# Performance work log

Measured on AMD Instinct MI355X. Metric: run time of the kernel, lower is better.

The kernel has to match this reference:

```python
import jax, jax.numpy as jnp
import numpy as np

N = 131072      # 8192 sudoku puzzles x 16 cells
E = 1048576     # random constraint edges (avg degree 8)
HID = 64
NEG_SLOPE = 0.2


def setup_inputs() -> dict:
    key = jax.random.key(0)
    ks = jax.random.split(key, 18)
    p = lambda k, shape: jax.random.normal(k, shape, dtype=jnp.float32) * 0.05
    return {
        "x": jax.random.randint(ks[0], (N,), 0, 5),
        "edge_index": jax.random.randint(ks[1], (2, E), 0, N),
        "emb": p(ks[2], (5, HID)),
        # conv1: in 64 -> heads=4, C=64, concat
        "W1": p(ks[3], (HID, 4 * HID)),
        "a1_src": p(ks[4], (4, HID)),
        "a1_dst": p(ks[5], (4, HID)),
        "b1": p(ks[6], (4 * HID,)),
        # conv2: in 256 -> heads=4, C=64, concat
        "W2": p(ks[7], (4 * HID, 4 * HID)),
        "a2_src": p(ks[8], (4, HID)),
        "a2_dst": p(ks[9], (4, HID)),
        "b2": p(ks[10], (4 * HID,)),
        # conv3: in 256 -> heads=1, C=64, no concat
        "W3": p(ks[11], (4 * HID, HID)),
        "a3_src": p(ks[12], (1, HID)),
        "a3_dst": p(ks[13], (1, HID)),
        "b3": p(ks[14], (HID,)),
        "fc_w": p(ks[15], (HID, 5)),
        "fc_b": p(ks[16], (5,)),
    }


def gat_conv(x, src, dst, W, a_src, a_dst, b, concat):
    """PyG-style GATConv (self-loops already appended to src/dst)."""
    n = x.shape[0]
    H, C = a_src.shape
    h = (x @ W).reshape(n, H, C)                       # [N,H,C]
    alpha_s = jnp.einsum('nhc,hc->nh', h, a_src)       # [N,H]
    alpha_d = jnp.einsum('nhc,hc->nh', h, a_dst)
    e = jax.nn.leaky_relu(alpha_s[src] + alpha_d[dst], NEG_SLOPE)  # [E,H]
    # scatter-softmax over incoming edges per destination node
    e_max = jax.ops.segment_max(e, dst, num_segments=n)
    e_exp = jnp.exp(e - e_max[dst])
    denom = jax.ops.segment_sum(e_exp, dst, num_segments=n)
    alpha = e_exp / (denom[dst] + 1e-16)               # [E,H]
    msg = h[src] * alpha[:, :, None]                   # [E,H,C]
    out = jax.ops.segment_sum(msg, dst, num_segments=n)  # [N,H,C]
    out = out.reshape(n, H * C) if concat else out.mean(axis=1)
    return out + b


def reference(x, edge_index, emb, W1, a1_src, a1_dst, b1,
              W2, a2_src, a2_dst, b2, W3, a3_src, a3_dst, b3, fc_w, fc_b):
    n = x.shape[0]
    loops = jnp.arange(n)
    src = jnp.concatenate([edge_index[0], loops])  # add self-loops (PyG default)
    dst = jnp.concatenate([edge_index[1], loops])
    h = emb[x]                                                    # [N,64]
    h = jax.nn.elu(gat_conv(h, src, dst, W1, a1_src, a1_dst, b1, True))
    h = jax.nn.elu(gat_conv(h, src, dst, W2, a2_src, a2_dst, b2, True))
    h = jax.nn.elu(gat_conv(h, src, dst, W3, a3_src, a3_dst, b3, False))
    return h @ fc_w + fc_b                                        # [N,5]
```

## Files before the change

kernel.cpp:

```cpp
#include <hip/hip_runtime.h>
#include <hip/hip_bf16.h>
#include <hip/hip_fp8.h>

typedef __attribute__((ext_vector_type(8))) short short8;
typedef __attribute__((ext_vector_type(4))) short short4_t;
typedef __attribute__((ext_vector_type(4))) float floatx4;
typedef __attribute__((ext_vector_type(2))) float floatx2;

constexpr int NB  = 256;
constexpr int CAP = 6144;

__device__ __forceinline__ unsigned short f2bf(float f){
  unsigned int u = __float_as_uint(f);
  u += 0x7FFF + ((u >> 16) & 1);
  return (unsigned short)(u >> 16);
}
__device__ __forceinline__ float bf2f(unsigned short h){
  return __uint_as_float(((unsigned int)h) << 16);
}
__device__ __forceinline__ float lrelu(float x){ return x > 0.f ? x : 0.2f * x; }
__device__ __forceinline__ float eluf(float x){ return x > 0.f ? x : (__expf(x) - 1.f); }

__device__ __forceinline__ unsigned char f2fp8(float f){
  __hip_fp8_e4m3 t(f);
  return (unsigned char)t.__x;
}
__device__ __forceinline__ float fp82f(unsigned char b){
  __hip_fp8_e4m3 t;
  t.__x = (__hip_fp8_storage_t)b;
  return (float)t;
}

template<bool HI>
__device__ __forceinline__ floatx2 fp8pk2(unsigned int v){
#if defined(__has_builtin) && __has_builtin(__builtin_amdgcn_cvt_pk_f32_fp8)
  return __builtin_amdgcn_cvt_pk_f32_fp8((int)v, HI);
#else
  floatx2 r;
  constexpr int sh = HI ? 16 : 0;
  r.x = fp82f((unsigned char)((v >> sh) & 0xFF));
  r.y = fp82f((unsigned char)((v >> (sh + 8)) & 0xFF));
  return r;
#endif
}

__device__ __forceinline__ unsigned int f32x4_to_fp8(float a0, float a1, float a2, float a3){
#if defined(__has_builtin) && __has_builtin(__builtin_amdgcn_cvt_pk_fp8_f32)
  int w = 0;
  w = __builtin_amdgcn_cvt_pk_fp8_f32(a0, a1, w, false);
  w = __builtin_amdgcn_cvt_pk_fp8_f32(a2, a3, w, true);
  return (unsigned int)w;
#else
  return (unsigned int)f2fp8(a0) | ((unsigned int)f2fp8(a1) << 8) |
         ((unsigned int)f2fp8(a2) << 16) | ((unsigned int)f2fp8(a3) << 24);
#endif
}

__device__ __forceinline__ int scr512(int p){
  int q = p >> 2, s = p & 3;
  int qq = ((q & 31) << 2) | (q >> 5);
  return (qq << 2) | s;
}

__device__ __forceinline__ void gload16(const unsigned short* g, unsigned short* l){
  __builtin_amdgcn_global_load_lds(
      (const __attribute__((address_space(1))) unsigned int*)(const void*)g,
      (__attribute__((address_space(3))) unsigned int*)(void*)l,
      16, 0, 0);
}

__global__ __launch_bounds__(256) void part_prep_k(const int* __restrict__ ei, int E, int shift,
                                                   const int* __restrict__ x,
                                                   int* __restrict__ gcnt,
                                                   unsigned* __restrict__ bbuf, int PB,
                                                   const float* __restrict__ W2,
                                                   unsigned short* __restrict__ Wp2,
                                                   const float* __restrict__ W3,
                                                   unsigned short* __restrict__ Wp3,
                                                   const float* __restrict__ emb,
                                                   const float* __restrict__ W1,
                                                   const float* __restrict__ a1s,
                                                   const float* __restrict__ a1d,
                                                   float* __restrict__ T1,
                                                   float* __restrict__ wt_tab){
  int blk = blockIdx.x;
  int tid = threadIdx.x;
  if (blk < PB){
    __shared__ int hist[NB];
    __shared__ int base[NB];
    hist[tid] = 0;
    __syncthreads();
    int blk_start = blk * 4096;
    int ldmask = (1 << shift) - 1;
    unsigned word[16];
    int bkt[16], lp[16];
    #pragma unroll
    for (int k = 0; k < 16; k++){
      int i = blk_start + k * 256 + tid;
      if (i < E){
        int dst = ei[E + i];
        int s = ei[i];
        int xs = x[s];
        bkt[k] = dst >> shift;
        word[k] = (unsigned)s | ((unsigned)(dst & ldmask) << 17) | ((unsigned)xs << 26);
        lp[k] = atomicAdd(&hist[bkt[k]], 1);
      } else {
        bkt[k] = -1;
      }
    }
    __syncthreads();
    base[tid] = atomicAdd(&gcnt[tid], hist[tid]);
    __syncthreads();
    #pragma unroll
    for (int k = 0; k < 16; k++){
      if (bkt[k] >= 0){
        int b = bkt[k];
        bbuf[(size_t)b * CAP + base[b] + lp[k]] = word[k];
      }
    }
    return;
  }
  int b = blk - PB;
  if (b < 256){
    int idx = b * 256 + tid;
    int k = idx >> 8, nn = idx & 255;
    Wp2[nn * 256 + k] = f2bf(W2[idx]);
  } else if (b < 320){
    int idx = (b - 256) * 256 + tid;
    int k = idx >> 6, nn = idx & 63;
    Wp3[nn * 256 + k] = f2bf(W3[idx]);
  } else {
    __shared__ float t_lds[1280];
    __shared__ float as_l[20], ad_l[20];
    for (int i = tid; i < 1280; i += 256){
      int r = i >> 8, c = i & 255;
      float s = 0.f;
      for (int k = 0; k < 64; k++) s += emb[r * 64 + k] * W1[k * 256 + c];
      t_lds[i] = s;
      T1[i] = s;
    }
    __syncthreads();
    if (tid < 20){
      int r = tid >> 2, hh = tid & 3;
      float ss = 0.f, sd = 0.f;
      for (int c = 0; c < 64; c++){
        float f = t_lds[r * 256 + hh * 64 + c];
        ss += f * a1s[hh * 64 + c];
        sd += f * a1d[hh * 64 + c];
      }
      as_l[tid] = ss;
      ad_l[tid] = sd;
    }
    __syncthreads();
    if (tid < 100){
      int xd = tid / 20, rest = tid % 20;
      int h = rest & 3;
      wt_tab[tid] = __expf(lrelu(as_l[rest] + ad_l[xd * 4 + h]));
    }
  }
}

__global__ __launch_bounds__(256) void bscan_k(const int* __restrict__ gcnt,
                                               int* __restrict__ gbase,
                                               int* __restrict__ row_ptr, int N, int dpb){
  __shared__ int s[NB];
  int t = threadIdx.x;
  int v = gcnt[t] + dpb;
  s[t] = v;
  __syncthreads();
  #pragma unroll
  for (int off = 1; off < NB; off <<= 1){
    int u = (t >= off) ? s[t - off] : 0;
    __syncthreads();
    s[t] += u;
    __syncthreads();
  }
  gbase[t] = s[t] - v;
  if (t == NB - 1){ gbase[NB] = s[t]; row_ptr[N] = s[t]; }
}

__global__ __launch_bounds__(256) void sort_k(const unsigned* __restrict__ bbuf,
                                              const int* __restrict__ gcnt,
                                              const int* __restrict__ gbase,
                                              const int* __restrict__ x,
                                              int* __restrict__ row_ptr,
                                              int* __restrict__ sorted_src,
                                              int* __restrict__ perm,
                                              uint2* __restrict__ cnt5, int dpb){
  __shared__ int counts[512];
  __shared__ int curs[512];
  __shared__ int wsum[256];
  __shared__ int sortedL[CAP + 512];
  __shared__ int dh[64];
  __shared__ int h5[512 * 5];
  int b = blockIdx.x, tid = threadIdx.x;
  int cnt = gcnt[b];
  int dstBase = b * dpb;
  int gb = gbase[b];
  counts[tid] = 0;
  counts[tid + 256] = 0;
  for (int i = tid; i < dpb * 5; i += 256) h5[i] = 0;
  __syncthreads();
  for (int i = tid; i < cnt; i += 256){
    unsigned pw = bbuf[(size_t)b * CAP + i];
    atomicAdd(&counts[(pw >> 17) & (dpb - 1)], 1);
  }
  {
    int x0 = x[dstBase + 2 * tid];
    int x1 = x[dstBase + 2 * tid + 1];
    atomicAdd(&h5[(2 * tid) * 5 + x0], 1);
    atomicAdd(&h5[(2 * tid + 1) * 5 + x1], 1);
  }
  __syncthreads();
  int c0 = counts[2 * tid] + 1;
  int c1 = counts[2 * tid + 1] + 1;
  int sum = c0 + c1;
  wsum[tid] = sum;
  __syncthreads();
  #pragma unroll
  for (int off = 1; off < 256; off <<= 1){
    int u = (tid >= off) ? wsum[tid - off] : 0;
    __syncthreads();
    wsum[tid] += u;
    __syncthreads();
  }
  int ex = wsum[tid] - sum;
  int ro0 = ex, ro1 = ex + c0;
  curs[2 * tid] = ro0 + 1;
  curs[2 * tid + 1] = ro1 + 1;
  sortedL[ro0] = dstBase + 2 * tid;
  sortedL[ro1] = dstBase + 2 * tid + 1;
  row_ptr[dstBase + 2 * tid] = gb + ro0;
  row_ptr[dstBase + 2 * tid + 1] = gb + ro1;
  __syncthreads();
  for (int i = tid; i < cnt; i += 256){
    unsigned pw = bbuf[(size_t)b * CAP + i];
    int ldst = (pw >> 17) & (dpb - 1);
    int pos = atomicAdd(&curs[ldst], 1);
    sortedL[pos] = (int)(pw & 0x1FFFF);
    atomicAdd(&h5[ldst * 5 + (pw >> 26)], 1);
  }
  __syncthreads();
  int tot = cnt + dpb;
  for (int i = tid; i < tot; i += 256) sorted_src[gb + i] = sortedL[i];

  {
    int d0 = 2 * tid, d1 = 2 * tid + 1;
    unsigned lo0 = (unsigned)h5[d0 * 5 + 0] | ((unsigned)h5[d0 * 5 + 1] << 8) |
                   ((unsigned)h5[d0 * 5 + 2] << 16) | ((unsigned)h5[d0 * 5 + 3] << 24);
    unsigned lo1 = (unsigned)h5[d1 * 5 + 0] | ((unsigned)h5[d1 * 5 + 1] << 8) |
                   ((unsigned)h5[d1 * 5 + 2] << 16) | ((unsigned)h5[d1 * 5 + 3] << 24);
    cnt5[dstBase + d0] = make_uint2(lo0, (unsigned)h5[d0 * 5 + 4]);
    cnt5[dstBase + d1] = make_uint2(lo1, (unsigned)h5[d1 * 5 + 4]);
  }

  __syncthreads();
  if (tid < 64) dh[tid] = 0;
  __syncthreads();
  int dg0 = c0 < 63 ? c0 : 63;
  int dg1 = c1 < 63 ? c1 : 63;
  int r0 = atomicAdd(&dh[dg0], 1);
  int r1 = atomicAdd(&dh[dg1], 1);
  __syncthreads();
  if (tid == 0){
    int run = 0;
    for (int i = 0; i < 64; i++){ int c = dh[i]; dh[i] = run; run += c; }
  }
  __syncthreads();
  perm[dstBase + scr512(dh[dg0] + r0)] = dstBase + 2 * tid;
  perm[dstBase + scr512(dh[dg1] + r1)] = dstBase + 2 * tid + 1;
}

template<int BN, int MODE, bool F8OUT>
__global__ __launch_bounds__(256) void gemm_lds_k(const unsigned short* __restrict__ A,
                                                  const unsigned short* __restrict__ Wp,
                                                  void* __restrict__ Cout, int Nc,
                                                  const float* __restrict__ a_src,
                                                  const float* __restrict__ a_dst,
                                                  float* __restrict__ as_arr,
                                                  float* __restrict__ ad_arr){
  constexpr int K = 256;
  constexpr int NT = BN / 32;
  __shared__ unsigned short Alds[128 * 32];
  __shared__ unsigned short Blds[BN * 32];
  __shared__ float asl[128], adl[128];
  __shared__ float pas[128][2], pad[128][2];
  int tid = threadIdx.x;
  int w = tid >> 6, l = tid & 63;
  int r16 = l & 15, quad = l >> 4;
  int wr = w >> 1, wc = w & 1;
  int mBase = blockIdx.x * 128;
  int nBase = blockIdx.y * BN;

  if constexpr (MODE == 1){
    if (tid < 128){ asl[tid] = a_src[nBase + tid]; adl[tid] = a_dst[nBase + tid]; }
  }
  if constexpr (MODE == 2){
    if (tid < 64){ asl[tid] = a_src[tid]; adl[tid] = a_dst[tid]; }
  }

  int arow = l >> 2;
  int kcol = (l & 3) * 8;
  const unsigned short* gA0 = A + (size_t)(mBase + w * 32 + arow) * K + kcol;
  const unsigned short* gA1 = gA0 + (size_t)16 * K;
  unsigned short* lA0 = &Alds[(w * 32) * 32];
  unsigned short* lA1 = &Alds[(w * 32 + 16) * 32];
  const unsigned short* gB0;
  const unsigned short* gB1 = nullptr;
  unsigned short* lB0;
  unsigned short* lB1 = nullptr;
  if constexpr (BN == 128){
    gB0 = Wp + (size_t)(nBase + w * 32 + arow) * K + kcol;
    gB1 = gB0 + (size_t)16 * K;
    lB0 = &Blds[(w * 32) * 32];
    lB1 = &Blds[(w * 32 + 16) * 32];
  } else {
    gB0 = Wp + (size_t)(nBase + w * 16 + arow) * K + kcol;
    lB0 = &Blds[(w * 16) * 32];
  }

  floatx4 acc[4][NT];
  #pragma unroll
  for (int mt = 0; mt < 4; mt++)
    #pragma unroll
    for (int nt = 0; nt < NT; nt++){ floatx4 z = {0.f,0.f,0.f,0.f}; acc[mt][nt] = z; }

  for (int kt = 0; kt < 8; kt++){
    int ko = kt * 32;
    gload16(gA0 + ko, lA0);
    gload16(gA1 + ko, lA1);
    gload16(gB0 + ko, lB0);
    if constexpr (BN == 128) gload16(gB1 + ko, lB1);
    __syncthreads();
    short8 af[4], bfr[NT];
    #pragma unroll
    for (int mt = 0; mt < 4; mt++)
      af[mt] = *(const short8*)&Alds[(wr * 64 + mt * 16 + r16) * 32 + quad * 8];
    #pragma unroll
    for (int nt = 0; nt < NT; nt++)
      bfr[nt] = *(const short8*)&Blds[(wc * (BN / 2) + nt * 16 + r16) * 32 + quad * 8];
    #pragma unroll
    for (int mt = 0; mt < 4; mt++)
      #pragma unroll
      for (int nt = 0; nt < NT; nt++)
        acc[mt][nt] = __builtin_amdgcn_mfma_f32_16x16x32_bf16(af[mt], bfr[nt], acc[mt][nt], 0, 0, 0);
    __syncthreads();
  }

  #pragma unroll
  for (int mt = 0; mt < 4; mt++){
    #pragma unroll
    for (int nt = 0; nt < NT; nt++){
      if constexpr (F8OUT){
        unsigned int pk = f32x4_to_fp8(acc[mt][nt][0] * 64.f, acc[mt][nt][1] * 64.f,
                                       acc[mt][nt][2] * 64.f, acc[mt][nt][3] * 64.f);
        int col = nBase + wc * (BN / 2) + nt * 16 + r16;
        int row0 = mBase + wr * 64 + mt * 16 + quad * 4;
        #pragma unroll
        for (int r = 0; r < 4; r++)
          ((unsigned char*)Cout)[(size_t)(row0 + r) * Nc + col] =
              (unsigned char)((pk >> (r * 8)) & 0xFF);
      } else {
        #pragma unroll
        for (int r = 0; r < 4; r++){
          int row = mBase + wr * 64 + mt * 16 + quad * 4 + r;
          int col = nBase + wc * (BN / 2) + nt * 16 + r16;
          ((unsigned short*)Cout)[(size_t)row * Nc + col] = f2bf(acc[mt][nt][r]);
        }
      }
    }
  }
  if constexpr (MODE == 1){
    int head = (nBase + wc * 64) >> 6;
    #pragma unroll
    for (int mt = 0; mt < 4; mt++){
      #pragma unroll
      for (int r = 0; r < 4; r++){
        float ps = 0.f, pd = 0.f;
        #pragma unroll
        for (int nt = 0; nt < NT; nt++){
          float v = acc[mt][nt][r];
          int ci = wc * 64 + nt * 16 + r16;
          ps += v * asl[ci];
          pd += v * adl[ci];
        }
        ps += __shfl_xor(ps, 1, 64); ps += __shfl_xor(ps, 2, 64);
        ps += __shfl_xor(ps, 4, 64); ps += __shfl_xor(ps, 8, 64);
        pd += __shfl_xor(pd, 1, 64); pd += __shfl_xor(pd, 2, 64);
        pd += __shfl_xor(pd, 4, 64); pd += __shfl_xor(pd, 8, 64);
        if (r16 == 0){
          int row = mBase + wr * 64 + mt * 16 + quad * 4 + r;
          as_arr[row * 4 + head] = ps;
          ad_arr[row * 4 + head] = pd;
        }
      }
    }
  }
  if constexpr (MODE == 2){
    #pragma unroll
    for (int mt = 0; mt < 4; mt++){
      #pragma unroll
      for (int r = 0; r < 4; r++){
        float ps = 0.f, pd = 0.f;
        #pragma unroll
        for (int nt = 0; nt < NT; nt++){
          float v = acc[mt][nt][r];
          int ci = wc * 32 + nt * 16 + r16;
          ps += v * asl[ci];
          pd += v * adl[ci];
        }
        ps += __shfl_xor(ps, 1, 64); ps += __shfl_xor(ps, 2, 64);
        ps += __shfl_xor(ps, 4, 64); ps += __shfl_xor(ps, 8, 64);
        pd += __shfl_xor(pd, 1, 64); pd += __shfl_xor(pd, 2, 64);
        pd += __shfl_xor(pd, 4, 64); pd += __shfl_xor(pd, 8, 64);
        if (r16 == 0){
          int lr = wr * 64 + mt * 16 + quad * 4 + r;
          pas[lr][wc] = ps;
          pad[lr][wc] = pd;
        }
      }
    }
    __syncthreads();
    if (tid < 128){
      as_arr[mBase + tid] = pas[tid][0] + pas[tid][1];
      ad_arr[mBase + tid] = pad[tid][0] + pad[tid][1];
    }
  }
}


__global__ __launch_bounds__(256) void agg1_k(const int* __restrict__ x,
                                              const float* __restrict__ T1,
                                              const float* __restrict__ wt_tab,
                                              const uint2* __restrict__ cnt5,
                                              const float* __restrict__ bias,
                                              unsigned short* __restrict__ outb){
  __shared__ float t_lds[1280];
  __shared__ float wt_l[100], b_lds[256];
  __shared__ float cnt_lds[256][5];
  __shared__ int xd_lds[256];
  int tid = threadIdx.x;
  for (int i = tid; i < 1280; i += 256) t_lds[i] = T1[i];
  if (tid < 100) wt_l[tid] = wt_tab[tid];
  b_lds[tid] = bias[tid];
  int d = blockIdx.x * 256 + tid;
  uint2 cw = cnt5[d];
  xd_lds[tid] = x[d];
  cnt_lds[tid][0] = (float)(cw.x & 0xFF);
  cnt_lds[tid][1] = (float)((cw.x >> 8) & 0xFF);
  cnt_lds[tid][2] = (float)((cw.x >> 16) & 0xFF);
  cnt_lds[tid][3] = (float)(cw.x >> 24);
  cnt_lds[tid][4] = (float)(cw.y & 0xFF);
  __syncthreads();
  int w = tid >> 6, l = tid & 63;
  int head = l >> 4;
  int c0i = l * 4;
  for (int dl = w; dl < 256; dl += 4){
    int dd = blockIdx.x * 256 + dl;
    int xd20 = xd_lds[dl] * 20;
    float ws[5];
    float den = 0.f;
    #pragma unroll
    for (int v2 = 0; v2 < 5; v2++){
      float wv = wt_l[xd20 + v2 * 4 + head] * cnt_lds[dl][v2];
      ws[v2] = wv;
      den += wv;
    }
    float inv = 1.f / (den + 1e-16f);
    float num[4] = {0.f, 0.f, 0.f, 0.f};
    #pragma unroll
    for (int v2 = 0; v2 < 5; v2++){
      const float4 row = *(const float4*)&t_lds[v2 * 256 + c0i];
      num[0] += ws[v2] * row.x;
      num[1] += ws[v2] * row.y;
      num[2] += ws[v2] * row.z;
      num[3] += ws[v2] * row.w;
    }
    short4_t ov;
    #pragma unroll
    for (int j = 0; j < 4; j++)
      ov[j] = (short)f2bf(eluf(num[j] * inv + b_lds[c0i + j]));
    *(short4_t*)(outb + (size_t)dd * 256 + c0i) = ov;
  }
}


__global__ __launch_bounds__(256) void agg4_k(const unsigned char* __restrict__ h8,
                                              const float* __restrict__ as_arr,
                                              const float* __restrict__ ad_arr,
                                              const int* __restrict__ row_ptr,
                                              const int* __restrict__ sorted_src,
                                              const int* __restrict__ perm,
                                              const float* __restrict__ bias,
                                              unsigned short* __restrict__ outb){
  int tid = threadIdx.x;
  int w = tid >> 6, l = tid & 63;
  int g = l >> 4, q = l & 15;
  int d = perm[blockIdx.x * 16 + w * 4 + g];
  unsigned coff = (unsigned)(q * 16);
  int head = q >> 2;
  int start = row_ptr[d], end = row_ptr[d + 1];
  float a_d = ad_arr[d * 4 + head];
  floatx2 ac[8];
  #pragma unroll
  for (int j = 0; j < 8; j++){ floatx2 z = {0.f, 0.f}; ac[j] = z; }
  float den = 0.f;
  int e = start;
  for (; e + 3 < end; e += 4){
    unsigned s0 = (unsigned)sorted_src[e];
    unsigned s1 = (unsigned)sorted_src[e + 1];
    unsigned s2 = (unsigned)sorted_src[e + 2];
    unsigned s3 = (unsigned)sorted_src[e + 3];
    uint4 v0 = *(const uint4*)(h8 + (((size_t)s0 << 8) | coff));
    uint4 v1 = *(const uint4*)(h8 + (((size_t)s1 << 8) | coff));
    uint4 v2 = *(const uint4*)(h8 + (((size_t)s2 << 8) | coff));
    uint4 v3 = *(const uint4*)(h8 + (((size_t)s3 << 8) | coff));
    float w0 = __expf(lrelu(as_arr[(s0 << 2) + head] + a_d));
    float w1 = __expf(lrelu(as_arr[(s1 << 2) + head] + a_d));
    float w2 = __expf(lrelu(as_arr[(s2 << 2) + head] + a_d));
    float w3 = __expf(lrelu(as_arr[(s3 << 2) + head] + a_d));
    den += (w0 + w1) + (w2 + w3);
    floatx2 W0 = {w0, w0}, W1 = {w1, w1}, W2 = {w2, w2}, W3 = {w3, w3};
    ac[0] += W0 * fp8pk2<false>(v0.x) + W1 * fp8pk2<false>(v1.x)
           + W2 * fp8pk2<false>(v2.x) + W3 * fp8pk2<false>(v3.x);
    ac[1] += W0 * fp8pk2<true>(v0.x)  + W1 * fp8pk2<true>(v1.x)
           + W2 * fp8pk2<true>(v2.x)  + W3 * fp8pk2<true>(v3.x);
    ac[2] += W0 * fp8pk2<false>(v0.y) + W1 * fp8pk2<false>(v1.y)
           + W2 * fp8pk2<false>(v2.y) + W3 * fp8pk2<false>(v3.y);
    ac[3] += W0 * fp8pk2<true>(v0.y)  + W1 * fp8pk2<true>(v1.y)
           + W2 * fp8pk2<true>(v2.y)  + W3 * fp8pk2<true>(v3.y);
    ac[4] += W0 * fp8pk2<false>(v0.z) + W1 * fp8pk2<false>(v1.z)
           + W2 * fp8pk2<false>(v2.z) + W3 * fp8pk2<false>(v3.z);
    ac[5] += W0 * fp8pk2<true>(v0.z)  + W1 * fp8pk2<true>(v1.z)
           + W2 * fp8pk2<true>(v2.z)  + W3 * fp8pk2<true>(v3.z);
    ac[6] += W0 * fp8pk2<false>(v0.w) + W1 * fp8pk2<false>(v1.w)
           + W2 * fp8pk2<false>(v2.w) + W3 * fp8pk2<false>(v3.w);
    ac[7] += W0 * fp8pk2<true>(v0.w)  + W1 * fp8pk2<true>(v1.w)
           + W2 * fp8pk2<true>(v2.w)  + W3 * fp8pk2<true>(v3.w);
  }
  for (; e < end; e++){
    unsigned s = (unsigned)sorted_src[e];
    uint4 v = *(const uint4*)(h8 + (((size_t)s << 8) | coff));
    float wg = __expf(lrelu(as_arr[(s << 2) + head] + a_d));
    den += wg;
    floatx2 wv = {wg, wg};
    ac[0] += wv * fp8pk2<false>(v.x);
    ac[1] += wv * fp8pk2<true>(v.x);
    ac[2] += wv * fp8pk2<false>(v.y);
    ac[3] += wv * fp8pk2<true>(v.y);
    ac[4] += wv * fp8pk2<false>(v.z);
    ac[5] += wv * fp8pk2<true>(v.z);
    ac[6] += wv * fp8pk2<false>(v.w);
    ac[7] += wv * fp8pk2<true>(v.w);
  }
  float inv = 0.015625f / (den + 1e-16f);
  int cb = q * 16;
  float4 bv0 = *(const float4*)&bias[cb];
  float4 bv1 = *(const float4*)&bias[cb + 4];
  float4 bv2 = *(const float4*)&bias[cb + 8];
  float4 bv3 = *(const float4*)&bias[cb + 12];
  float bb[16] = {bv0.x, bv0.y, bv0.z, bv0.w, bv1.x, bv1.y, bv1.z, bv1.w,
                  bv2.x, bv2.y, bv2.z, bv2.w, bv3.x, bv3.y, bv3.z, bv3.w};
  short8 o0, o1;
  #pragma unroll
  for (int j = 0; j < 8; j++){
    float v = ((j & 1) ? ac[j >> 1].y : ac[j >> 1].x);
    o0[j] = (short)f2bf(eluf(v * inv + bb[j]));
  }
  #pragma unroll
  for (int j = 0; j < 8; j++){
    float v = ((j & 1) ? ac[4 + (j >> 1)].y : ac[4 + (j >> 1)].x);
    o1[j] = (short)f2bf(eluf(v * inv + bb[8 + j]));
  }
  *(short8*)(outb + (size_t)d * 256 + cb) = o0;
  *(short8*)(outb + (size_t)d * 256 + cb + 8) = o1;
}


__global__ __launch_bounds__(256) void agg3_k(const unsigned char* __restrict__ h8,
                                              const float* __restrict__ as_arr,
                                              const float* __restrict__ ad_arr,
                                              const int* __restrict__ row_ptr,
                                              const int* __restrict__ sorted_src,
                                              const int* __restrict__ perm,
                                              const float* __restrict__ bias,
                                              const float* __restrict__ fcw,
                                              const float* __restrict__ fcb,
                                              float* __restrict__ out){
  __shared__ float w_lds[320];
  __shared__ float fb5[5];
  int tid = threadIdx.x;
  for (int i = tid; i < 320; i += 256) w_lds[i] = fcw[i];
  if (tid < 5) fb5[tid] = fcb[tid];
  __syncthreads();
  int w = tid >> 6, l = tid & 63;
  int g = l >> 3, q = l & 7;
  int d = perm[blockIdx.x * 32 + w * 8 + g];
  unsigned coff = (unsigned)(q * 8);
  int start = row_ptr[d], end = row_ptr[d + 1];
  float a_d = ad_arr[d];
  floatx2 ac[4];
  #pragma unroll
  for (int j = 0; j < 4; j++){ floatx2 z = {0.f, 0.f}; ac[j] = z; }
  float den = 0.f;
  int e = start;
  for (; e + 3 < end; e += 4){
    unsigned s0 = (unsigned)sorted_src[e];
    unsigned s1 = (unsigned)sorted_src[e + 1];
    unsigned s2 = (unsigned)sorted_src[e + 2];
    unsigned s3 = (unsigned)sorted_src[e + 3];
    uint2 v0 = *(const uint2*)(h8 + (((size_t)s0 << 6) | coff));
    uint2 v1 = *(const uint2*)(h8 + (((size_t)s1 << 6) | coff));
    uint2 v2 = *(const uint2*)(h8 + (((size_t)s2 << 6) | coff));
    uint2 v3 = *(const uint2*)(h8 + (((size_t)s3 << 6) | coff));
    float w0 = __expf(lrelu(as_arr[s0] + a_d));
    float w1 = __expf(lrelu(as_arr[s1] + a_d));
    float w2 = __expf(lrelu(as_arr[s2] + a_d));
    float w3 = __expf(lrelu(as_arr[s3] + a_d));
    den += (w0 + w1) + (w2 + w3);
    floatx2 W0 = {w0, w0}, W1 = {w1, w1}, W2 = {w2, w2}, W3 = {w3, w3};
    ac[0] += W0 * fp8pk2<false>(v0.x) + W1 * fp8pk2<false>(v1.x)
           + W2 * fp8pk2<false>(v2.x) + W3 * fp8pk2<false>(v3.x);
    ac[1] += W0 * fp8pk2<true>(v0.x)  + W1 * fp8pk2<true>(v1.x)
           + W2 * fp8pk2<true>(v2.x)  + W3 * fp8pk2<true>(v3.x);
    ac[2] += W0 * fp8pk2<false>(v0.y) + W1 * fp8pk2<false>(v1.y)
           + W2 * fp8pk2<false>(v2.y) + W3 * fp8pk2<false>(v3.y);
    ac[3] += W0 * fp8pk2<true>(v0.y)  + W1 * fp8pk2<true>(v1.y)
           + W2 * fp8pk2<true>(v2.y)  + W3 * fp8pk2<true>(v3.y);
  }
  for (; e < end; e++){
    unsigned s = (unsigned)sorted_src[e];
    float wg = __expf(lrelu(as_arr[s] + a_d));
    den += wg;
    uint2 v = *(const uint2*)(h8 + (((size_t)s << 6) | coff));
    floatx2 wv = {wg, wg};
    ac[0] += wv * fp8pk2<false>(v.x);
    ac[1] += wv * fp8pk2<true>(v.x);
    ac[2] += wv * fp8pk2<false>(v.y);
    ac[3] += wv * fp8pk2<true>(v.y);
  }
  float inv = 0.015625f / (den + 1e-16f);
  int cb = q * 8;
  float4 bA = *(const float4*)&bias[cb];
  float4 bB = *(const float4*)&bias[cb + 4];
  float bb[8] = {bA.x, bA.y, bA.z, bA.w, bB.x, bB.y, bB.z, bB.w};
  float p0 = 0.f, p1 = 0.f, p2 = 0.f, p3 = 0.f, p4 = 0.f;
  #pragma unroll
  for (int j = 0; j < 8; j++){
    float v = ((j & 1) ? ac[j >> 1].y : ac[j >> 1].x);
    float h = eluf(v * inv + bb[j]);
    const float* wr = &w_lds[(cb + j) * 5];
    p0 += h * wr[0];
    p1 += h * wr[1];
    p2 += h * wr[2];
    p3 += h * wr[3];
    p4 += h * wr[4];
  }
  p0 += __shfl_xor(p0, 1, 64); p0 += __shfl_xor(p0, 2, 64); p0 += __shfl_xor(p0, 4, 64);
  p1 += __shfl_xor(p1, 1, 64); p1 += __shfl_xor(p1, 2, 64); p1 += __shfl_xor(p1, 4, 64);
  p2 += __shfl_xor(p2, 1, 64); p2 += __shfl_xor(p2, 2, 64); p2 += __shfl_xor(p2, 4, 64);
  p3 += __shfl_xor(p3, 1, 64); p3 += __shfl_xor(p3, 2, 64); p3 += __shfl_xor(p3, 4, 64);
  p4 += __shfl_xor(p4, 1, 64); p4 += __shfl_xor(p4, 2, 64); p4 += __shfl_xor(p4, 4, 64);
  if (q == 0){
    float* o = out + (size_t)d * 5;
    o[0] = p0 + fb5[0];
    o[1] = p1 + fb5[1];
    o[2] = p2 + fb5[2];
    o[3] = p3 + fb5[3];
    o[4] = p4 + fb5[4];
  }
}


extern "C" void kernel_launch(void* const* d_in, const int* in_sizes, int n_in,
                              void* d_out, int out_size, void* d_ws, size_t ws_size,
                              hipStream_t stream){
  const int*   x    = (const int*)d_in[0];
  const int*   ei   = (const int*)d_in[1];
  const float* emb  = (const float*)d_in[2];
  const float* W1   = (const float*)d_in[3];
  const float* a1s  = (const float*)d_in[4];
  const float* a1d  = (const float*)d_in[5];
  const float* b1   = (const float*)d_in[6];
  const float* W2   = (const float*)d_in[7];
  const float* a2s  = (const float*)d_in[8];
  const float* a2d  = (const float*)d_in[9];
  const float* b2   = (const float*)d_in[10];
  const float* W3   = (const float*)d_in[11];
  const float* a3s  = (const float*)d_in[12];
  const float* a3d  = (const float*)d_in[13];
  const float* b3   = (const float*)d_in[14];
  const float* fcw  = (const float*)d_in[15];
  const float* fcb  = (const float*)d_in[16];
  float* out = (float*)d_out;

  const int N = in_sizes[0];
  const int E = in_sizes[1] / 2;
  const int dpb = N / NB;
  int shift = 0;
  while ((1 << shift) < dpb) shift++;
  const int PB = (E + 4095) / 4096;

  char* base = (char*)d_ws;
  size_t off = 0;
  auto alloc = [&](size_t bytes) -> void* {
    void* p = base + off;
    off += (bytes + 255) & ~(size_t)255;
    return p;
  };
  unsigned short* bufB    = (unsigned short*)alloc((size_t)N * 256 * 2);
  unsigned char*  buf8    = (unsigned char*)alloc((size_t)N * 256);
  float* alpha_s          = (float*)alloc((size_t)N * 4 * 4);
  float* alpha_d          = (float*)alloc((size_t)N * 4 * 4);
  int* row_ptr            = (int*)alloc((size_t)(N + 1) * 4);
  int* sorted_src         = (int*)alloc((size_t)(E + N) * 4);
  int* perm               = (int*)alloc((size_t)N * 4);
  uint2* cnt5             = (uint2*)alloc((size_t)N * 8);
  unsigned* bbuf          = (unsigned*)alloc((size_t)NB * CAP * 4);
  int* gcnt               = (int*)alloc((size_t)NB * 4);
  int* gbase              = (int*)alloc((size_t)(NB + 1) * 4);
  float* T1               = (float*)alloc(5 * 256 * 4);
  float* wt_tab           = (float*)alloc(100 * 4);
  unsigned short* Wp2     = (unsigned short*)alloc(256 * 256 * 2);
  unsigned short* Wp3     = (unsigned short*)alloc(64 * 256 * 2);

  (void)hipMemsetAsync(gcnt, 0, (size_t)NB * 4, stream);
  part_prep_k<<<PB + 321, 256, 0, stream>>>(ei, E, shift, x, gcnt, bbuf, PB,
                                            W2, Wp2, W3, Wp3, emb, W1, a1s, a1d, T1, wt_tab);
  bscan_k<<<1, 256, 0, stream>>>(gcnt, gbase, row_ptr, N, dpb);
  sort_k<<<NB, 256, 0, stream>>>(bbuf, gcnt, gbase, x, row_ptr, sorted_src, perm, cnt5, dpb);

  agg1_k<<<N / 256, 256, 0, stream>>>(x, T1, wt_tab, cnt5, b1, bufB);

  gemm_lds_k<128, 1, true><<<dim3(N / 128, 2), 256, 0, stream>>>(bufB, Wp2, buf8, 256,
                                                                 a2s, a2d, alpha_s, alpha_d);
  agg4_k<<<N / 16, 256, 0, stream>>>(buf8, alpha_s, alpha_d, row_ptr, sorted_src, perm, b2, bufB);

  gemm_lds_k<64, 2, true><<<dim3(N / 128, 1), 256, 0, stream>>>(bufB, Wp3, buf8, 64,
                                                                a3s, a3d, alpha_s, alpha_d);
  agg3_k<<<N / 32, 256, 0, stream>>>(buf8, alpha_s, alpha_d, row_ptr, sorted_src, perm, b3,
                                     fcw, fcb, out);
}
```

Measured before the change: 310.6 us.

## Fuse layer-3 projection GEMM into layer-2 aggregation epilogue

The layer-2 aggregation kernel now keeps its 16 output rows in LDS and multiplies them right away by W3 with bf16 MFMA. It writes the fp8 layer-3 features and the per-node attention logits directly, so the separate layer-3 GEMM launch and the bf16 round trip of the 256-wide hidden state through global memory go away. In exchange, every block reloads the full 64x256 W3 into about 34 KB of LDS, which may lower occupancy of the latency-bound gather kernel. The scr512 swizzle helper is also rewritten, perhaps to match a different layout.

Result: slower. 325.8 us (+4.9%).

```diff
diff --git a/kernel.cpp b/kernel.cpp
--- a/kernel.cpp
+++ b/kernel.cpp
@@ -57,9 +57,9 @@
 }
 
 __device__ __forceinline__ int scr512(int p){
-  int q = p >> 2, s = p & 3;
-  int qq = ((q & 31) << 2) | (q >> 5);
-  return (qq << 2) | s;
+  int c = p >> 4, s = p & 15;
+  int cc = ((c & 7) << 2) | (c >> 3);
+  return (cc << 4) | s;
 }
 
 __device__ __forceinline__ void gload16(const unsigned short* g, unsigned short* l){
@@ -485,18 +485,39 @@
 }
 
 
-__global__ __launch_bounds__(256) void agg4_k(const unsigned char* __restrict__ h8,
-                                              const float* __restrict__ as_arr,
-                                              const float* __restrict__ ad_arr,
-                                              const int* __restrict__ row_ptr,
-                                              const int* __restrict__ sorted_src,
-                                              const int* __restrict__ perm,
-                                              const float* __restrict__ bias,
-                                              unsigned short* __restrict__ outb){
+__global__ __launch_bounds__(256) void agg4g_k(const unsigned char* __restrict__ h8,
+                                               const float* __restrict__ as_arr,
+                                               const float* __restrict__ ad_arr,
+                                               const int* __restrict__ row_ptr,
+                                               const int* __restrict__ sorted_src,
+                                               const int* __restrict__ perm,
+                                               const float* __restrict__ bias,
+                                               const unsigned short* __restrict__ Wp3,
+                                               const float* __restrict__ a3s,
+                                               const float* __restrict__ a3d,
+                                               unsigned char* __restrict__ h3out,
+                                               float* __restrict__ as3,
+                                               float* __restrict__ ad3){
+  constexpr int LDK = 264;
+  __shared__ unsigned short hlds[16 * LDK];
+  __shared__ unsigned short w3lds[64 * LDK];
+  __shared__ float pasl[16][4], padl[16][4];
+  __shared__ unsigned char h3st[16 * 64];
+  __shared__ int dlds[16];
   int tid = threadIdx.x;
   int w = tid >> 6, l = tid & 63;
   int g = l >> 4, q = l & 15;
-  int d = perm[blockIdx.x * 16 + w * 4 + g];
+  int rr = w * 4 + g;
+  int d = perm[blockIdx.x * 16 + rr];
+  if (q == 0) dlds[rr] = d;
+
+  #pragma unroll
+  for (int i = 0; i < 8; i++){
+    int c = i * 256 + tid;
+    int row = c >> 5, col8 = (c & 31) << 3;
+    *(short8*)&w3lds[row * LDK + col8] = *(const short8*)&Wp3[row * 256 + col8];
+  }
+
   unsigned coff = (unsigned)(q * 16);
   int head = q >> 2;
   int start = row_ptr[d], end = row_ptr[d + 1];
@@ -572,8 +593,49 @@
     float v = ((j & 1) ? ac[4 + (j >> 1)].y : ac[4 + (j >> 1)].x);
     o1[j] = (short)f2bf(eluf(v * inv + bb[8 + j]));
   }
-  *(short8*)(outb + (size_t)d * 256 + cb) = o0;
-  *(short8*)(outb + (size_t)d * 256 + cb + 8) = o1;
+  *(short8*)&hlds[rr * LDK + cb] = o0;
+  *(short8*)&hlds[rr * LDK + cb + 8] = o1;
+  __syncthreads();
+
+  int r16 = l & 15, quad = l >> 4;
+  floatx4 acc3 = {0.f, 0.f, 0.f, 0.f};
+  #pragma unroll
+  for (int kt = 0; kt < 8; kt++){
+    short8 af = *(const short8*)&hlds[r16 * LDK + kt * 32 + quad * 8];
+    short8 bf = *(const short8*)&w3lds[(w * 16 + r16) * LDK + kt * 32 + quad * 8];
+    acc3 = __builtin_amdgcn_mfma_f32_16x16x32_bf16(af, bf, acc3, 0, 0, 0);
+  }
+  float a3sv = a3s[w * 16 + r16];
+  float a3dv = a3d[w * 16 + r16];
+  float ps[4], pd[4];
+  #pragma unroll
+  for (int r = 0; r < 4; r++){
+    ps[r] = acc3[r] * a3sv;
+    pd[r] = acc3[r] * a3dv;
+    ps[r] += __shfl_xor(ps[r], 1, 64); ps[r] += __shfl_xor(ps[r], 2, 64);
+    ps[r] += __shfl_xor(ps[r], 4, 64); ps[r] += __shfl_xor(ps[r], 8, 64);
+    pd[r] += __shfl_xor(pd[r], 1, 64); pd[r] += __shfl_xor(pd[r], 2, 64);
+    pd[r] += __shfl_xor(pd[r], 4, 64); pd[r] += __shfl_xor(pd[r], 8, 64);
+    h3st[(quad * 4 + r) * 64 + w * 16 + r16] = f2fp8(acc3[r] * 64.f);
+  }
+  if (r16 == 0){
+    #pragma unroll
+    for (int r = 0; r < 4; r++){
+      pasl[quad * 4 + r][w] = ps[r];
+      padl[quad * 4 + r][w] = pd[r];
+    }
+  }
+  __syncthreads();
+  {
+    int row = tid >> 4, c4 = tid & 15;
+    unsigned v = *(const unsigned*)&h3st[row * 64 + c4 * 4];
+    int dd = dlds[row];
+    *(unsigned*)(h3out + (size_t)dd * 64 + c4 * 4) = v;
+    if (c4 == 0){
+      as3[dd] = pasl[row][0] + pasl[row][1] + pasl[row][2] + pasl[row][3];
+      ad3[dd] = padl[row][0] + padl[row][1] + padl[row][2] + padl[row][3];
+    }
+  }
 }
 
 
@@ -710,8 +772,11 @@
   };
   unsigned short* bufB    = (unsigned short*)alloc((size_t)N * 256 * 2);
   unsigned char*  buf8    = (unsigned char*)alloc((size_t)N * 256);
+  unsigned char*  buf8b   = (unsigned char*)alloc((size_t)N * 64);
   float* alpha_s          = (float*)alloc((size_t)N * 4 * 4);
   float* alpha_d          = (float*)alloc((size_t)N * 4 * 4);
+  float* as3              = (float*)alloc((size_t)N * 4);
+  float* ad3              = (float*)alloc((size_t)N * 4);
   int* row_ptr            = (int*)alloc((size_t)(N + 1) * 4);
   int* sorted_src         = (int*)alloc((size_t)(E + N) * 4);
   int* perm               = (int*)alloc((size_t)N * 4);
@@ -734,10 +799,9 @@
 
   gemm_lds_k<128, 1, true><<<dim3(N / 128, 2), 256, 0, stream>>>(bufB, Wp2, buf8, 256,
                                                                  a2s, a2d, alpha_s, alpha_d);
-  agg4_k<<<N / 16, 256, 0, stream>>>(buf8, alpha_s, alpha_d, row_ptr, sorted_src, perm, b2, bufB);
-
-  gemm_lds_k<64, 2, true><<<dim3(N / 128, 1), 256, 0, stream>>>(bufB, Wp3, buf8, 64,
-                                                                a3s, a3d, alpha_s, alpha_d);
-  agg3_k<<<N / 32, 256, 0, stream>>>(buf8, alpha_s, alpha_d, row_ptr, sorted_src, perm, b3,
+  agg4g_k<<<N / 16, 256, 0, stream>>>(buf8, alpha_s, alpha_d, row_ptr, sorted_src, perm, b2,
+                                      Wp3, a3s, a3d, buf8b, as3, ad3);
+
+  agg3_k<<<N / 32, 256, 0, stream>>>(buf8b, as3, ad3, row_ptr, sorted_src, perm, b3,
                                      fcw, fcb, out);
 }
```
